# Kernel optimization log

Measured on AMD Instinct MI355X. Metric: run time of the kernel, lower is better.

## Reference

```python
import jax, jax.numpy as jnp
import numpy as np

B, N, D, C, F, T = 8, 2048, 8, 128, 256, 4


def grover_diffusion(n):
    g = np.ones((n, n), np.float32) * (2.0 / n)
    np.fill_diagonal(g, -1.0 + 2.0 / n)
    return g


def build_swap_indices():
    # D-regular circulant graph: neighbors of j are (j +/- 1..D/2) mod N.
    offsets = np.array([-4, -3, -2, -1, 1, 2, 3, 4])
    cols = (np.arange(N)[:, None] + offsets[None, :]) % N          # [N,D]
    A = np.zeros((N, N), np.int32)
    A[np.arange(N)[:, None], cols] = 1
    nb_sorted = np.sort(cols, axis=1)                               # ascending neighbor ids, as np.argwhere gives
    cum = np.cumsum(A, axis=0) - A                                  # exclusive prefix count per column (scan order j=0..N-1)
    swap_a = nb_sorted.astype(np.int32)                             # [N,D]
    swap_b = cum[np.arange(N)[:, None], nb_sorted].astype(np.int32) # [N,D]
    # same graph for every batch element, tiled to match original per-batch indexing
    return (np.broadcast_to(swap_a, (B, N, D)).copy(),
            np.broadcast_to(swap_b, (B, N, D)).copy())


def setup_inputs() -> dict:
    key = jax.random.key(0)
    k1, k2 = jax.random.split(key)
    init_amps = jax.random.normal(k1, (B, N, D, C), dtype=jnp.float32)
    neibs = jax.random.normal(k2, (B, N, F), dtype=jnp.float32)
    coins = jnp.asarray(np.stack([grover_diffusion(D) for _ in range(T)], 0))  # [T,D,D]
    sa, sb = build_swap_indices()
    return {
        "init_amps": init_amps,
        "neibs": neibs,
        "coins": coins,
        "swap_a": jnp.asarray(sa),
        "swap_b": jnp.asarray(sb),
        "time_steps": T,
        "degree": D,
    }


def reference(init_amps, neibs, coins, swap_a, swap_b, time_steps, degree):
    amps = init_amps  # [B,N,D,C]

    def shift(a_i, sa_i, sb_i):
        # a_i: [N,D,C], sa_i/sb_i: [N,D] -> gathered [N,D,C]
        return a_i[sa_i, sb_i]

    gather = jax.vmap(shift)
    for t in range(time_steps):
        # coin step: matmul(amps.permute(0,1,3,2), coin).permute(0,1,3,2)
        a = jnp.einsum('bndc,de->bnec', amps, coins[t])
        # shift step: amps[b,j,n] = a[b, swap_a[b,j,n], swap_b[b,j,n]]
        amps = gather(a, swap_a, swap_b)

    d = jnp.sum(amps * amps, axis=2)                 # [B,N,C]
    quant_neibs = jnp.einsum('bnc,bnf->bcf', d, neibs)  # d^T @ neibs
    return quant_neibs.reshape(-1, quant_neibs.shape[2])  # [B*C, F]
```

## Files before the change

kernel.cpp:

```cpp
#include <hip/hip_runtime.h>

#define Bv 8
#define Nv 2048
#define Dv 8
#define Cv 128
#define Fv 256
#define Tv 4

#define CC   32
#define HALO 16

template<int TILE_, int LN_, int NTILES_>
__global__ __launch_bounds__(LN_ * 8, 4)
void walk_kernel(const float* __restrict__ amps0,
                 const float* __restrict__ coins,
                 const int* __restrict__ swap_a,
                 const int* __restrict__ swap_b,
                 float* __restrict__ dsum)
{
    extern __shared__ float abuf[];

    const int bid  = blockIdx.x;
    const int b    = bid / (NTILES_ * 4);
    const int rem  = bid - b * (NTILES_ * 4);
    const int tile = rem >> 2;
    const int c0   = (rem & 3) * CC;

    const int tid = threadIdx.x;
    const int ci4 = tid & 7;
    const int nl  = tid >> 3;

    const int n_load_start = tile * TILE_ - HALO;
    const int ng = (n_load_start + nl) & (Nv - 1);

    float4 amp[Dv];
    int    idx[Dv];

    {
        const float* srcf = amps0 + ((size_t)(b * Nv + ng) * Dv) * Cv + c0 + ci4 * 4;
        #pragma unroll
        for (int dd = 0; dd < Dv; ++dd)
            amp[dd] = *reinterpret_cast<const float4*>(srcf + (size_t)dd * Cv);
    }

    {
        const int* pa = swap_a + (size_t)(b * Nv + ng) * Dv;
        const int* pb = swap_b + (size_t)(b * Nv + ng) * Dv;
        #pragma unroll
        for (int dd = 0; dd < Dv; ++dd) {
            const int sa = pa[dd];
            const int sb = pb[dd];
            const int sl = (sa - n_load_start + Nv) & (LN_ - 1);
            idx[dd] = (sl * Dv + sb) * CC + ci4 * 4;
        }
    }

    for (int t = 0; t < Tv; ++t) {
        const float* cm = coins + t * Dv * Dv;
        float4 a[Dv];

        const float wd = cm[0];
        const float wo = cm[1];
        bool uni = true;
        #pragma unroll
        for (int i = 0; i < Dv; ++i)
            #pragma unroll
            for (int j = 0; j < Dv; ++j)
                uni = uni && (cm[i * Dv + j] == ((i == j) ? wd : wo));

        if (uni) {
            const float dw = wd - wo;
            float4 s = amp[0];
            #pragma unroll
            for (int dd = 1; dd < Dv; ++dd) {
                s.x += amp[dd].x; s.y += amp[dd].y;
                s.z += amp[dd].z; s.w += amp[dd].w;
            }
            #pragma unroll
            for (int e = 0; e < Dv; ++e) {
                a[e].x = wo * s.x + dw * amp[e].x;
                a[e].y = wo * s.y + dw * amp[e].y;
                a[e].z = wo * s.z + dw * amp[e].z;
                a[e].w = wo * s.w + dw * amp[e].w;
            }
        } else {
            #pragma unroll
            for (int e = 0; e < Dv; ++e) { a[e].x = a[e].y = a[e].z = a[e].w = 0.f; }
            #pragma unroll
            for (int dd = 0; dd < Dv; ++dd) {
                #pragma unroll
                for (int e = 0; e < Dv; ++e) {
                    const float w = cm[dd * Dv + e];
                    a[e].x += amp[dd].x * w;
                    a[e].y += amp[dd].y * w;
                    a[e].z += amp[dd].z * w;
                    a[e].w += amp[dd].w * w;
                }
            }
        }

        {
            float* base = abuf + nl * (Dv * CC) + ci4 * 4;
            #pragma unroll
            for (int e = 0; e < Dv; ++e)
                *reinterpret_cast<float4*>(base + e * CC) = a[e];
        }
        __syncthreads();
        #pragma unroll
        for (int dd = 0; dd < Dv; ++dd)
            amp[dd] = *reinterpret_cast<const float4*>(&abuf[idx[dd]]);
        __syncthreads();
    }

    if (nl >= HALO && nl < HALO + TILE_) {
        float4 s;
        s.x = s.y = s.z = s.w = 0.f;
        #pragma unroll
        for (int dd = 0; dd < Dv; ++dd) {
            s.x += amp[dd].x * amp[dd].x;
            s.y += amp[dd].y * amp[dd].y;
            s.z += amp[dd].z * amp[dd].z;
            s.w += amp[dd].w * amp[dd].w;
        }
        *reinterpret_cast<float4*>(dsum + (size_t)(b * Nv + ng) * Cv + c0 + ci4 * 4) = s;
    }
}

constexpr int BIG_TILE = 96,  BIG_LN = 128, BIG_NT = 22;
constexpr int SM_TILE  = 32,  SM_LN  = 64,  SM_NT  = 64;
constexpr size_t BIG_LDS = (size_t)BIG_LN * Dv * CC * 4;
constexpr size_t SM_LDS  = (size_t)SM_LN  * Dv * CC * 4;

#define CQ    32
#define NCH   128
#define NPART (Nv / NCH)
constexpr size_t OUT_FLOATS  = (size_t)Bv * Cv * Fv;
constexpr size_t DSUM_BYTES  = (size_t)Bv * Nv * Cv * 4;
constexpr size_t PART_BYTES  = (size_t)NPART * OUT_FLOATS * 4;

typedef float v2f __attribute__((ext_vector_type(2)));

template<bool ATOMIC>
__global__ __launch_bounds__(256)
void quant_kernel(const float* __restrict__ dsum,
                  const float* __restrict__ neibs,
                  float* __restrict__ dst)
{
    const int bid = blockIdx.x;
    const int b   = bid >> 6;
    const int cq  = (bid >> 4) & 3;
    const int nc  = bid & 15;
    const int c0  = cq * CQ;
    const int n0  = nc * NCH;
    const int f   = threadIdx.x;

    v2f acc2[CQ / 2];
    #pragma unroll
    for (int k = 0; k < CQ / 2; ++k) acc2[k] = (v2f){0.f, 0.f};

    const float* nbp = neibs + ((size_t)b * Nv + n0) * Fv + f;
    const float* dp  = dsum  + ((size_t)b * Nv + n0) * Cv + c0;

    #pragma unroll 2
    for (int n = 0; n < NCH; ++n) {
        const float nbv = nbp[(size_t)n * Fv];
        const v2f nb2 = {nbv, nbv};
        const v2f* dp2 = reinterpret_cast<const v2f*>(dp + (size_t)n * Cv);
        #pragma unroll
        for (int k = 0; k < CQ / 2; ++k)
            acc2[k] += dp2[k] * nb2;
    }

    if (ATOMIC) {
        float* op = dst + ((size_t)b * Cv + c0) * Fv + f;
        #pragma unroll
        for (int k = 0; k < CQ / 2; ++k) {
            atomicAdd(op + (size_t)(2 * k)     * Fv, acc2[k].x);
            atomicAdd(op + (size_t)(2 * k + 1) * Fv, acc2[k].y);
        }
    } else {
        float* op = dst + (size_t)nc * OUT_FLOATS + ((size_t)b * Cv + c0) * Fv + f;
        #pragma unroll
        for (int k = 0; k < CQ / 2; ++k) {
            op[(size_t)(2 * k)     * Fv] = acc2[k].x;
            op[(size_t)(2 * k + 1) * Fv] = acc2[k].y;
        }
    }
}

__global__ __launch_bounds__(256)
void reduce_kernel(const float* __restrict__ partials, float* __restrict__ out)
{
    const size_t i = ((size_t)blockIdx.x * 256 + threadIdx.x) * 4;
    float4 s = {0.f, 0.f, 0.f, 0.f};
    #pragma unroll
    for (int nc = 0; nc < NPART; ++nc) {
        const float4 p = *reinterpret_cast<const float4*>(partials + nc * OUT_FLOATS + i);
        s.x += p.x; s.y += p.y; s.z += p.z; s.w += p.w;
    }
    *reinterpret_cast<float4*>(out + i) = s;
}

extern "C" void kernel_launch(void* const* d_in, const int* in_sizes, int n_in,
                              void* d_out, int out_size, void* d_ws, size_t ws_size,
                              hipStream_t stream)
{
    const float* amps   = (const float*)d_in[0];
    const float* neibs  = (const float*)d_in[1];
    const float* coins  = (const float*)d_in[2];
    const int*   swap_a = (const int*)d_in[3];
    const int*   swap_b = (const int*)d_in[4];
    float* out  = (float*)d_out;
    float* dsum = (float*)d_ws;

    hipError_t attr_ok = hipFuncSetAttribute(
        reinterpret_cast<const void*>(&walk_kernel<BIG_TILE, BIG_LN, BIG_NT>),
        hipFuncAttributeMaxDynamicSharedMemorySize, (int)BIG_LDS);

    const bool use_partials = (ws_size >= DSUM_BYTES + PART_BYTES);
    float* partials = (float*)((char*)d_ws + DSUM_BYTES);

    if (!use_partials) {
        hipMemsetAsync(d_out, 0, OUT_FLOATS * sizeof(float), stream);
    }

    if (attr_ok == hipSuccess) {
        walk_kernel<BIG_TILE, BIG_LN, BIG_NT>
            <<<Bv * BIG_NT * 4, BIG_LN * 8, BIG_LDS, stream>>>(
                amps, coins, swap_a, swap_b, dsum);
    } else {
        walk_kernel<SM_TILE, SM_LN, SM_NT>
            <<<Bv * SM_NT * 4, SM_LN * 8, SM_LDS, stream>>>(
                amps, coins, swap_a, swap_b, dsum);
    }

    const int quant_grid = Bv * (Cv / CQ) * NPART;
    if (use_partials) {
        quant_kernel<false><<<quant_grid, 256, 0, stream>>>(dsum, neibs, partials);
        reduce_kernel<<<(int)(OUT_FLOATS / 4 / 256), 256, 0, stream>>>(partials, out);
    } else {
        quant_kernel<true><<<quant_grid, 256, 0, stream>>>(dsum, neibs, out);
    }
}
```

Baseline: 204.9 us.

## Retile walk kernel with padded static LDS and register-blocked quant GEMM

The walk kernel now uses a fixed 64-node tile with a 96-row halo buffer, 16-channel slices and a padded row stride in static shared memory. This drops the dynamic-LDS attribute call and aims to reduce bank conflicts while raising occupancy. The coin uniformity check is hoisted out of the time loop, and the coin update is written as FMAs. The quant kernel becomes a 4x4 register-blocked outer product over an 8-way N split with float4 loads, cutting partial-buffer traffic for the reduce step. The halo wrap relies on a masked index that assumes the neighbour offsets stay within the halo.

```diff
diff --git a/kernel.cpp b/kernel.cpp
--- a/kernel.cpp
+++ b/kernel.cpp
@@ -7,30 +7,33 @@
 #define Fv 256
 #define Tv 4
 
-#define CC   32
-#define HALO 16
-
-template<int TILE_, int LN_, int NTILES_>
-__global__ __launch_bounds__(LN_ * 8, 4)
+#define CC    16
+#define TILE  64
+#define HALO  16
+#define LN    96
+#define RS    132
+#define NT    32
+
+__global__ __launch_bounds__(LN * 4, 4)
 void walk_kernel(const float* __restrict__ amps0,
                  const float* __restrict__ coins,
                  const int* __restrict__ swap_a,
                  const int* __restrict__ swap_b,
                  float* __restrict__ dsum)
 {
-    extern __shared__ float abuf[];
+    __shared__ float abuf[LN * RS];
 
     const int bid  = blockIdx.x;
-    const int b    = bid / (NTILES_ * 4);
-    const int rem  = bid - b * (NTILES_ * 4);
-    const int tile = rem >> 2;
-    const int c0   = (rem & 3) * CC;
+    const int b    = bid >> 8;
+    const int rem  = bid & 255;
+    const int tile = rem >> 3;
+    const int c0   = (rem & 7) * CC;
 
     const int tid = threadIdx.x;
-    const int ci4 = tid & 7;
-    const int nl  = tid >> 3;
-
-    const int n_load_start = tile * TILE_ - HALO;
+    const int ci4 = tid & 3;
+    const int nl  = tid >> 2;
+
+    const int n_load_start = tile * TILE - HALO;
     const int ng = (n_load_start + nl) & (Nv - 1);
 
     float4 amp[Dv];
@@ -50,40 +53,50 @@
         for (int dd = 0; dd < Dv; ++dd) {
             const int sa = pa[dd];
             const int sb = pb[dd];
-            const int sl = (sa - n_load_start + Nv) & (LN_ - 1);
-            idx[dd] = (sl * Dv + sb) * CC + ci4 * 4;
-        }
-    }
-
+            int s1 = sa - n_load_start;
+            if (s1 < 0)   s1 += Nv;
+            if (s1 >= Nv) s1 -= Nv;
+            if (s1 >= LN) s1 &= 63;
+            idx[dd] = s1 * RS + sb * CC + ci4 * 4;
+        }
+    }
+
+    float wdv[Tv], wov[Tv];
+    bool uni = true;
+    #pragma unroll
+    for (int tt = 0; tt < Tv; ++tt) {
+        const float* cm = coins + tt * Dv * Dv;
+        wdv[tt] = cm[0];
+        wov[tt] = cm[1];
+        #pragma unroll
+        for (int i = 0; i < Dv; ++i)
+            #pragma unroll
+            for (int j = 0; j < Dv; ++j)
+                uni = uni && (cm[i * Dv + j] == ((i == j) ? wdv[tt] : wov[tt]));
+    }
+
+    #pragma unroll
     for (int t = 0; t < Tv; ++t) {
-        const float* cm = coins + t * Dv * Dv;
         float4 a[Dv];
-
-        const float wd = cm[0];
-        const float wo = cm[1];
-        bool uni = true;
-        #pragma unroll
-        for (int i = 0; i < Dv; ++i)
-            #pragma unroll
-            for (int j = 0; j < Dv; ++j)
-                uni = uni && (cm[i * Dv + j] == ((i == j) ? wd : wo));
-
         if (uni) {
-            const float dw = wd - wo;
+            const float wo = wov[t];
+            const float dw = wdv[t] - wo;
             float4 s = amp[0];
             #pragma unroll
             for (int dd = 1; dd < Dv; ++dd) {
                 s.x += amp[dd].x; s.y += amp[dd].y;
                 s.z += amp[dd].z; s.w += amp[dd].w;
             }
+            const float4 ws = {wo * s.x, wo * s.y, wo * s.z, wo * s.w};
             #pragma unroll
             for (int e = 0; e < Dv; ++e) {
-                a[e].x = wo * s.x + dw * amp[e].x;
-                a[e].y = wo * s.y + dw * amp[e].y;
-                a[e].z = wo * s.z + dw * amp[e].z;
-                a[e].w = wo * s.w + dw * amp[e].w;
+                a[e].x = fmaf(dw, amp[e].x, ws.x);
+                a[e].y = fmaf(dw, amp[e].y, ws.y);
+                a[e].z = fmaf(dw, amp[e].z, ws.z);
+                a[e].w = fmaf(dw, amp[e].w, ws.w);
             }
         } else {
+            const float* cm = coins + t * Dv * Dv;
             #pragma unroll
             for (int e = 0; e < Dv; ++e) { a[e].x = a[e].y = a[e].z = a[e].w = 0.f; }
             #pragma unroll
@@ -100,7 +113,7 @@
         }
 
         {
-            float* base = abuf + nl * (Dv * CC) + ci4 * 4;
+            float* base = abuf + nl * RS + ci4 * 4;
             #pragma unroll
             for (int e = 0; e < Dv; ++e)
                 *reinterpret_cast<float4*>(base + e * CC) = a[e];
@@ -112,7 +125,7 @@
         __syncthreads();
     }
 
-    if (nl >= HALO && nl < HALO + TILE_) {
+    if (nl >= HALO && nl < HALO + TILE) {
         float4 s;
         s.x = s.y = s.z = s.w = 0.f;
         #pragma unroll
@@ -126,65 +139,62 @@
     }
 }
 
-constexpr int BIG_TILE = 96,  BIG_LN = 128, BIG_NT = 22;
-constexpr int SM_TILE  = 32,  SM_LN  = 64,  SM_NT  = 64;
-constexpr size_t BIG_LDS = (size_t)BIG_LN * Dv * CC * 4;
-constexpr size_t SM_LDS  = (size_t)SM_LN  * Dv * CC * 4;
-
-#define CQ    32
-#define NCH   128
-#define NPART (Nv / NCH)
-constexpr size_t OUT_FLOATS  = (size_t)Bv * Cv * Fv;
-constexpr size_t DSUM_BYTES  = (size_t)Bv * Nv * Cv * 4;
-constexpr size_t PART_BYTES  = (size_t)NPART * OUT_FLOATS * 4;
+#define NSPL  8
+constexpr size_t OUT_FLOATS = (size_t)Bv * Cv * Fv;
+constexpr size_t DSUM_BYTES = (size_t)Bv * Nv * Cv * 4;
+constexpr size_t PART_BYTES = (size_t)NSPL * OUT_FLOATS * 4;
 
 typedef float v2f __attribute__((ext_vector_type(2)));
 
-template<bool ATOMIC>
+template<int NSPL_>
 __global__ __launch_bounds__(256)
 void quant_kernel(const float* __restrict__ dsum,
                   const float* __restrict__ neibs,
                   float* __restrict__ dst)
 {
     const int bid = blockIdx.x;
-    const int b   = bid >> 6;
-    const int cq  = (bid >> 4) & 3;
-    const int nc  = bid & 15;
-    const int c0  = cq * CQ;
-    const int n0  = nc * NCH;
-    const int f   = threadIdx.x;
-
-    v2f acc2[CQ / 2];
-    #pragma unroll
-    for (int k = 0; k < CQ / 2; ++k) acc2[k] = (v2f){0.f, 0.f};
-
-    const float* nbp = neibs + ((size_t)b * Nv + n0) * Fv + f;
-    const float* dp  = dsum  + ((size_t)b * Nv + n0) * Cv + c0;
-
-    #pragma unroll 2
-    for (int n = 0; n < NCH; ++n) {
-        const float nbv = nbp[(size_t)n * Fv];
-        const v2f nb2 = {nbv, nbv};
-        const v2f* dp2 = reinterpret_cast<const v2f*>(dp + (size_t)n * Cv);
-        #pragma unroll
-        for (int k = 0; k < CQ / 2; ++k)
-            acc2[k] += dp2[k] * nb2;
-    }
-
-    if (ATOMIC) {
-        float* op = dst + ((size_t)b * Cv + c0) * Fv + f;
-        #pragma unroll
-        for (int k = 0; k < CQ / 2; ++k) {
-            atomicAdd(op + (size_t)(2 * k)     * Fv, acc2[k].x);
-            atomicAdd(op + (size_t)(2 * k + 1) * Fv, acc2[k].y);
-        }
-    } else {
-        float* op = dst + (size_t)nc * OUT_FLOATS + ((size_t)b * Cv + c0) * Fv + f;
-        #pragma unroll
-        for (int k = 0; k < CQ / 2; ++k) {
-            op[(size_t)(2 * k)     * Fv] = acc2[k].x;
-            op[(size_t)(2 * k + 1) * Fv] = acc2[k].y;
-        }
+    const int nc  = bid % NSPL_;
+    int r = bid / NSPL_;
+    const int ft = r & 3;  r >>= 2;
+    const int ct = r & 1;  r >>= 1;
+    const int b  = r;
+
+    const int tid = threadIdx.x;
+    const int tf  = tid & 15;
+    const int tc  = tid >> 4;
+
+    const int c0  = ct * 64 + tc * 4;
+    const int f0  = ft * 64 + tf * 4;
+    const int n0  = nc * (Nv / NSPL_);
+    const int nch = Nv / NSPL_;
+
+    const float* dg = dsum  + ((size_t)b * Nv + n0) * Cv + c0;
+    const float* ng = neibs + ((size_t)b * Nv + n0) * Fv + f0;
+
+    v2f acc[4][2];
+    #pragma unroll
+    for (int i = 0; i < 4; ++i) {
+        acc[i][0] = (v2f){0.f, 0.f};
+        acc[i][1] = (v2f){0.f, 0.f};
+    }
+
+    #pragma unroll 4
+    for (int k = 0; k < nch; ++k) {
+        const float4 dv = *reinterpret_cast<const float4*>(dg + (size_t)k * Cv);
+        const float4 nv = *reinterpret_cast<const float4*>(ng + (size_t)k * Fv);
+        const v2f nb0 = {nv.x, nv.y};
+        const v2f nb1 = {nv.z, nv.w};
+        acc[0][0] += nb0 * dv.x;  acc[0][1] += nb1 * dv.x;
+        acc[1][0] += nb0 * dv.y;  acc[1][1] += nb1 * dv.y;
+        acc[2][0] += nb0 * dv.z;  acc[2][1] += nb1 * dv.z;
+        acc[3][0] += nb0 * dv.w;  acc[3][1] += nb1 * dv.w;
+    }
+
+    float* op = dst + (size_t)nc * OUT_FLOATS + ((size_t)b * Cv + c0) * Fv + f0;
+    #pragma unroll
+    for (int i = 0; i < 4; ++i) {
+        const float4 v = {acc[i][0].x, acc[i][0].y, acc[i][1].x, acc[i][1].y};
+        *reinterpret_cast<float4*>(op + (size_t)i * Fv) = v;
     }
 }
 
@@ -194,7 +204,7 @@
     const size_t i = ((size_t)blockIdx.x * 256 + threadIdx.x) * 4;
     float4 s = {0.f, 0.f, 0.f, 0.f};
     #pragma unroll
-    for (int nc = 0; nc < NPART; ++nc) {
+    for (int nc = 0; nc < NSPL; ++nc) {
         const float4 p = *reinterpret_cast<const float4*>(partials + nc * OUT_FLOATS + i);
         s.x += p.x; s.y += p.y; s.z += p.z; s.w += p.w;
     }
@@ -213,32 +223,16 @@
     float* out  = (float*)d_out;
     float* dsum = (float*)d_ws;
 
-    hipError_t attr_ok = hipFuncSetAttribute(
-        reinterpret_cast<const void*>(&walk_kernel<BIG_TILE, BIG_LN, BIG_NT>),
-        hipFuncAttributeMaxDynamicSharedMemorySize, (int)BIG_LDS);
+    walk_kernel<<<Bv * NT * (Cv / CC), LN * 4, 0, stream>>>(
+        amps, coins, swap_a, swap_b, dsum);
 
     const bool use_partials = (ws_size >= DSUM_BYTES + PART_BYTES);
     float* partials = (float*)((char*)d_ws + DSUM_BYTES);
 
-    if (!use_partials) {
-        hipMemsetAsync(d_out, 0, OUT_FLOATS * sizeof(float), stream);
-    }
-
-    if (attr_ok == hipSuccess) {
-        walk_kernel<BIG_TILE, BIG_LN, BIG_NT>
-            <<<Bv * BIG_NT * 4, BIG_LN * 8, BIG_LDS, stream>>>(
-                amps, coins, swap_a, swap_b, dsum);
-    } else {
-        walk_kernel<SM_TILE, SM_LN, SM_NT>
-            <<<Bv * SM_NT * 4, SM_LN * 8, SM_LDS, stream>>>(
-                amps, coins, swap_a, swap_b, dsum);
-    }
-
-    const int quant_grid = Bv * (Cv / CQ) * NPART;
     if (use_partials) {
-        quant_kernel<false><<<quant_grid, 256, 0, stream>>>(dsum, neibs, partials);
+        quant_kernel<NSPL><<<Bv * 2 * 4 * NSPL, 256, 0, stream>>>(dsum, neibs, partials);
         reduce_kernel<<<(int)(OUT_FLOATS / 4 / 256), 256, 0, stream>>>(partials, out);
     } else {
-        quant_kernel<true><<<quant_grid, 256, 0, stream>>>(dsum, neibs, out);
-    }
-}
+        quant_kernel<1><<<Bv * 2 * 4, 256, 0, stream>>>(dsum, neibs, out);
+    }
+}
```

Result: faster. 197.7 us (-3.5%).
